# Optimization experiments

Measured on AMD Instinct MI355X. Metric: run time of the kernel, lower is better.

Reference implementation:

```python
import jax, jax.numpy as jnp
import numpy as np

HIDDEN = 768
HEADS = 12
HEAD_DIM = HIDDEN // HEADS


def setup_inputs() -> dict:
    key = jax.random.key(0)
    ks = jax.random.split(key, 9)
    B, S = 2, 2048
    scale = 1.0 / np.sqrt(HIDDEN)
    return {
        "hidden_states": jax.random.normal(ks[0], (B, S, HIDDEN), jnp.float32),
        "context": jax.random.normal(ks[1], (B, S, HIDDEN), jnp.float32),
        "attention_mask": jnp.zeros((B, 1, 1, S), jnp.float32),
        "Wq": jax.random.normal(ks[2], (HIDDEN, HIDDEN), jnp.float32) * scale,
        "bq": jnp.zeros((HIDDEN,), jnp.float32),
        "Wk": jax.random.normal(ks[3], (HIDDEN, HIDDEN), jnp.float32) * scale,
        "bk": jnp.zeros((HIDDEN,), jnp.float32),
        "Wv": jax.random.normal(ks[4], (HIDDEN, HIDDEN), jnp.float32) * scale,
        "bv": jnp.zeros((HIDDEN,), jnp.float32),
    }


def _split_heads(x):
    # [B, S, H*D] -> [B, H, S, D]
    B, S, _ = x.shape
    return x.reshape(B, S, HEADS, HEAD_DIM).transpose(0, 2, 1, 3)


def reference(hidden_states, context, attention_mask, Wq, bq, Wk, bk, Wv, bv):
    # torch Linear: y = x @ W^T + b
    q = _split_heads(hidden_states @ Wq.T + bq)   # [B,H,Sq,D]
    k = _split_heads(context @ Wk.T + bk)         # [B,H,Sk,D]
    v = _split_heads(context @ Wv.T + bv)         # [B,H,Sk,D]

    scores = jnp.einsum("bhqd,bhkd->bhqk", q, k)
    scores = scores / np.sqrt(HEAD_DIM + 1e-05)
    scores = scores + attention_mask
    probs = jax.nn.softmax(scores, axis=-1)       # dropout p=0 -> identity (eval)
    ctx = jnp.einsum("bhqk,bhkd->bhqd", probs, v) # [B,H,Sq,D]
    B, H, Sq, D = ctx.shape
    return ctx.transpose(0, 2, 1, 3).reshape(B, Sq, H * D)
```

## Files before the change

### kernel.cpp

```cpp
#include <hip/hip_runtime.h>
#include <hip/hip_bf16.h>
#include <math.h>

typedef short s16x8 __attribute__((ext_vector_type(8)));
typedef float f32x4 __attribute__((ext_vector_type(4)));
typedef _Float16 f16x4 __attribute__((ext_vector_type(4)));
typedef __fp16 fp16x2 __attribute__((ext_vector_type(2)));
typedef unsigned short u16;

#define NHEADS 12
#define SEQ 2048
#define NBH 24
#define KDIM 768
#define LOG2E 1.44269504088896f

#define SWZ(row, col) (((row) * 64) + ((col) ^ (((row) & 7) << 3)))

#define GLOAD_LDS16(g, l) __builtin_amdgcn_global_load_lds( \
    (const __attribute__((address_space(1))) unsigned int*)(g), \
    (__attribute__((address_space(3))) unsigned int*)(l), 16, 0, 0)

static __device__ __forceinline__ u16 f2bf(float f) {
    union { float f; unsigned u; } v; v.f = f;
    unsigned r = v.u + 0x7fffu + ((v.u >> 16) & 1u);
    return (u16)(r >> 16);
}
static __device__ __forceinline__ u16 f2h(float f) {
    union { _Float16 h; u16 u; } v; v.h = (_Float16)f;
    return v.u;
}
static __device__ __forceinline__ f16x4 pack4(float a, float b, float c, float d) {
    union { fp16x2 h2[2]; f16x4 h4; } u;
    u.h2[0] = __builtin_amdgcn_cvt_pkrtz(a, b);
    u.h2[1] = __builtin_amdgcn_cvt_pkrtz(c, d);
    return u.h4;
}

__global__ void cvt6_kernel(const float* __restrict__ s0, const float* __restrict__ s1,
                            const float* __restrict__ s2, const float* __restrict__ s3,
                            const float* __restrict__ s4, const float* __restrict__ s5,
                            u16* __restrict__ d0, u16* __restrict__ d1, u16* __restrict__ d2,
                            u16* __restrict__ d3, u16* __restrict__ d4, float* __restrict__ d5,
                            int n4a, int n4w, float qscl) {
    const int z = blockIdx.z;
    int i = blockIdx.x * blockDim.x + threadIdx.x;
    if (z == 5) {
        if (i < (2 * SEQ) / 4) {
            float4 f = ((const float4*)s5)[i];
            f.x *= LOG2E; f.y *= LOG2E; f.z *= LOG2E; f.w *= LOG2E;
            ((float4*)d5)[i] = f;
        }
        return;
    }
    const float* src = (z == 0) ? s0 : (z == 1) ? s1 : (z == 2) ? s2 : (z == 3) ? s3 : s4;
    u16* dst         = (z == 0) ? d0 : (z == 1) ? d1 : (z == 2) ? d2 : (z == 3) ? d3 : d4;
    const int n4     = (z < 2) ? n4a : n4w;
    const float scl  = (z == 2) ? qscl : 1.0f;
    if (i < n4) {
        float4 f = ((const float4*)src)[i];
        ushort4 o;
        o.x = f2bf(f.x * scl); o.y = f2bf(f.y * scl); o.z = f2bf(f.z * scl); o.w = f2bf(f.w * scl);
        ((ushort4*)dst)[i] = o;
    }
}

__launch_bounds__(256)
__global__ void qkv_gemm(const u16* __restrict__ X, const u16* __restrict__ C,
                         const u16* __restrict__ W0, const u16* __restrict__ W1, const u16* __restrict__ W2,
                         const float* __restrict__ b0, const float* __restrict__ b1, const float* __restrict__ b2,
                         u16* __restrict__ Qo, u16* __restrict__ Ko, u16* __restrict__ Vo, float qscl) {
    const int z = blockIdx.z;
    const u16* A    = (z == 0) ? X  : C;
    const u16* W    = (z == 0) ? W0 : (z == 1) ? W1 : W2;
    const float* bi = (z == 0) ? b0 : (z == 1) ? b1 : b2;
    u16* out        = (z == 0) ? Qo : (z == 1) ? Ko : Vo;
    const float bscl = (z == 0) ? qscl : 1.0f;

    __shared__ u16 As[3][4096];
    __shared__ u16 Bs[3][4096];

    const int tid  = threadIdx.x;
    const int lane = tid & 63;
    const int wid  = tid >> 6;
    const int wr = wid >> 1, wc = wid & 1;
    const int l15 = lane & 15, lh = lane >> 4;
    const int mBase = blockIdx.x * 128;
    const int nBase = blockIdx.y * 128;

    size_t aSrc[2], bSrc[2]; int ldsOff[2];
    #pragma unroll
    for (int i = 0; i < 2; ++i) {
        int L = i * 2048 + tid * 8;
        int prow = L >> 6;
        int pcol = (L & 63) ^ ((prow & 7) << 3);
        int row = (prow << 1) | (pcol >> 5);
        int col = pcol & 31;
        aSrc[i] = (size_t)(mBase + row) * KDIM + col;
        bSrc[i] = (size_t)(nBase + row) * KDIM + col;
        ldsOff[i] = i * 2048 + wid * 512;
    }

#define G_STAGE(step, buf) do { \
        const size_t kb_ = (size_t)(step) * 32; \
        GLOAD_LDS16(&A[aSrc[0] + kb_], &As[buf][ldsOff[0]]); \
        GLOAD_LDS16(&A[aSrc[1] + kb_], &As[buf][ldsOff[1]]); \
        GLOAD_LDS16(&W[bSrc[0] + kb_], &Bs[buf][ldsOff[0]]); \
        GLOAD_LDS16(&W[bSrc[1] + kb_], &Bs[buf][ldsOff[1]]); \
    } while (0)

    f32x4 acc[4][4] = {};

    G_STAGE(0, 0);
    G_STAGE(1, 1);

    const int NIT = KDIM / 32;
    int cur = 0;
    for (int it = 0; it < NIT; ++it) {
        if (it + 1 < NIT) asm volatile("s_waitcnt vmcnt(4)" ::: "memory");
        else              asm volatile("s_waitcnt vmcnt(0)" ::: "memory");
        __builtin_amdgcn_s_barrier();
        __builtin_amdgcn_sched_barrier(0);

        s16x8 xf[4], wf[4];
        #pragma unroll
        for (int m = 0; m < 4; ++m) {
            int row = wr * 64 + m * 16 + l15;
            xf[m] = *(const s16x8*)(&As[cur][SWZ(row >> 1, (row & 1) * 32 + lh * 8)]);
        }
        #pragma unroll
        for (int n = 0; n < 4; ++n) {
            int row = wc * 64 + n * 16 + l15;
            wf[n] = *(const s16x8*)(&Bs[cur][SWZ(row >> 1, (row & 1) * 32 + lh * 8)]);
        }
        if (z < 2) {
            #pragma unroll
            for (int m = 0; m < 4; ++m)
                #pragma unroll
                for (int n = 0; n < 4; ++n)
                    acc[m][n] = __builtin_amdgcn_mfma_f32_16x16x32_bf16(wf[n], xf[m], acc[m][n], 0, 0, 0);
        } else {
            #pragma unroll
            for (int m = 0; m < 4; ++m)
                #pragma unroll
                for (int n = 0; n < 4; ++n)
                    acc[m][n] = __builtin_amdgcn_mfma_f32_16x16x32_bf16(xf[m], wf[n], acc[m][n], 0, 0, 0);
        }

        if (it + 2 < NIT) {
            int nxt = cur + 2; if (nxt >= 3) nxt -= 3;
            G_STAGE(it + 2, nxt);
        }
        ++cur; if (cur == 3) cur = 0;
    }
#undef G_STAGE

    if (z < 2) {
        #pragma unroll
        for (int m = 0; m < 4; ++m) {
            int sg = mBase + wr * 64 + m * 16 + l15;
            int b = sg >> 11, s = sg & 2047;
            #pragma unroll
            for (int n = 0; n < 4; ++n) {
                int d0 = nBase + wc * 64 + n * 16 + lh * 4;
                int h = d0 >> 6, d = d0 & 63;
                float4 bv = *(const float4*)(&bi[d0]);
                ushort4 o;
                o.x = f2bf(acc[m][n][0] + bv.x * bscl);
                o.y = f2bf(acc[m][n][1] + bv.y * bscl);
                o.z = f2bf(acc[m][n][2] + bv.z * bscl);
                o.w = f2bf(acc[m][n][3] + bv.w * bscl);
                *(ushort4*)(&out[(((size_t)(b * NHEADS + h) * SEQ + s) << 6) + d]) = o;
            }
        }
    } else {
        #pragma unroll
        for (int m = 0; m < 4; ++m) {
            #pragma unroll
            for (int n = 0; n < 4; ++n) {
                int colg = nBase + wc * 64 + n * 16 + l15;
                float bv = bi[colg];
                int h = colg >> 6, d = colg & 63;
                int rowg0 = mBase + wr * 64 + m * 16 + lh * 4;
                int b = rowg0 >> 11, s = rowg0 & 2047;
                int sp = (s & ~0x3C) | (((s >> 2) & 3) << 4) | (((s >> 4) & 3) << 2);
                ushort4 o;
                o.x = f2h(acc[m][n][0] + bv);
                o.y = f2h(acc[m][n][1] + bv);
                o.z = f2h(acc[m][n][2] + bv);
                o.w = f2h(acc[m][n][3] + bv);
                *(ushort4*)(&out[(((size_t)(b * NHEADS + h) * 64 + d) << 11) + sp]) = o;
            }
        }
    }
}

template<bool SPLIT>
__launch_bounds__(512)
__global__ void attn_kernel(const u16* __restrict__ Qg, const u16* __restrict__ Kg,
                            const u16* __restrict__ Vg,
                            const float* __restrict__ maskL, float* __restrict__ out,
                            u16* __restrict__ OpartH, float* __restrict__ MLpart) {
    __shared__ u16 Ks[2][64 * 64];
    __shared__ u16 Vt[2][64 * 64];
    __shared__ float maskLds[2048];

    const int tid  = threadIdx.x;
    const int lane = tid & 63;
    const int wid  = tid >> 6;
    const int bh = blockIdx.y;
    const int b = bh / NHEADS;
    const int h = bh % NHEADS;
    const int q0 = blockIdx.x * 128 + wid * 16;
    const int l15 = lane & 15, lh = lane >> 4;
    const int z = SPLIT ? blockIdx.z : 0;
    const int NT = SPLIT ? (SEQ / 128) : (SEQ / 64);
    const int tile0 = z * NT;

    for (int i = tid * 4; i < NT * 64; i += 512 * 4)
        *(float4*)(&maskLds[i]) = *(const float4*)(&maskL[(size_t)b * SEQ + (tile0 << 6) + i]);

    const int srow = tid >> 3;
    const int scol = ((tid & 7) * 8) ^ ((srow & 7) << 3);
    const size_t kSrc = (((size_t)bh * SEQ + srow) << 6) + scol + ((size_t)tile0 << 12);
    const size_t vSrc = (((size_t)bh * 64 + srow) << 11) + scol + (size_t)tile0 * 64;
    const int ldsBase = wid * 512;

    s16x8 qf[2];
    #pragma unroll
    for (int kk = 0; kk < 2; ++kk)
        qf[kk] = *(const s16x8*)(&Qg[(((size_t)bh * SEQ + q0 + l15) << 6) + kk * 32 + lh * 8]);

    f32x4 oacc[4] = {};
    float mrun = -1e30f, lrun = 0.f;

    GLOAD_LDS16(&Kg[kSrc], &Ks[0][ldsBase]);
    GLOAD_LDS16(&Vg[vSrc], &Vt[0][ldsBase]);

    for (int t = 0; t < NT; ++t) {
        const int cur = t & 1;
        __syncthreads();
        if (t + 1 < NT) {
            GLOAD_LDS16(&Kg[kSrc + ((size_t)(t + 1) << 12)], &Ks[cur ^ 1][ldsBase]);
            GLOAD_LDS16(&Vg[vSrc + (size_t)(t + 1) * 64],    &Vt[cur ^ 1][ldsBase]);
        }

        f32x4 sacc[4];
        #pragma unroll
        for (int n = 0; n < 4; ++n) {
            float4 mv = *(const float4*)(&maskLds[t * 64 + n * 16 + lh * 4]);
            sacc[n][0] = mv.x; sacc[n][1] = mv.y; sacc[n][2] = mv.z; sacc[n][3] = mv.w;
        }
        __builtin_amdgcn_s_setprio(1);
        #pragma unroll
        for (int kk = 0; kk < 2; ++kk) {
            #pragma unroll
            for (int n = 0; n < 4; ++n) {
                s16x8 kf = *(const s16x8*)(&Ks[cur][SWZ(n * 16 + l15, kk * 32 + lh * 8)]);
                sacc[n] = __builtin_amdgcn_mfma_f32_16x16x32_bf16(kf, qf[kk], sacc[n], 0, 0, 0);
            }
        }
        __builtin_amdgcn_s_setprio(0);

        float tmax = sacc[0][0];
        #pragma unroll
        for (int n = 0; n < 4; ++n)
            #pragma unroll
            for (int j = 0; j < 4; ++j)
                tmax = fmaxf(tmax, sacc[n][j]);

        if (!__all(tmax - mrun <= 11.0f)) {
            float rmax = fmaxf(tmax, __shfl_xor(tmax, 16));
            rmax = fmaxf(rmax, __shfl_xor(rmax, 32));
            float mnew = fmaxf(mrun, rmax);
            float alpha = __builtin_amdgcn_exp2f(mrun - mnew);
            lrun *= alpha;
            #pragma unroll
            for (int nd = 0; nd < 4; ++nd)
                #pragma unroll
                for (int j = 0; j < 4; ++j)
                    oacc[nd][j] *= alpha;
            mrun = mnew;
        }

        f16x4 pf[4];
        #pragma unroll
        for (int n = 0; n < 4; ++n) {
            float p0 = __builtin_amdgcn_exp2f(sacc[n][0] - mrun);
            float p1 = __builtin_amdgcn_exp2f(sacc[n][1] - mrun);
            float p2 = __builtin_amdgcn_exp2f(sacc[n][2] - mrun);
            float p3 = __builtin_amdgcn_exp2f(sacc[n][3] - mrun);
            lrun += (p0 + p1) + (p2 + p3);
            pf[n] = pack4(p0, p1, p2, p3);
        }

        __builtin_amdgcn_s_setprio(1);
        #pragma unroll
        for (int kk = 0; kk < 2; ++kk) {
            #pragma unroll
            for (int nd = 0; nd < 4; ++nd) {
                s16x8 v2 = *(const s16x8*)(&Vt[cur][SWZ(nd * 16 + l15, lh * 16 + kk * 8)]);
                union { s16x8 s8; f16x4 h4[2]; } u; u.s8 = v2;
                oacc[nd] = __builtin_amdgcn_mfma_f32_16x16x16f16(u.h4[0], pf[2 * kk],     oacc[nd], 0, 0, 0);
                oacc[nd] = __builtin_amdgcn_mfma_f32_16x16x16f16(u.h4[1], pf[2 * kk + 1], oacc[nd], 0, 0, 0);
            }
        }
        __builtin_amdgcn_s_setprio(0);
    }

    lrun += __shfl_xor(lrun, 16);
    lrun += __shfl_xor(lrun, 32);

    const float inv = 1.0f / lrun;
    const int s = q0 + l15;
    if (!SPLIT) {
        #pragma unroll
        for (int nd = 0; nd < 4; ++nd) {
            float4 o;
            o.x = oacc[nd][0] * inv; o.y = oacc[nd][1] * inv;
            o.z = oacc[nd][2] * inv; o.w = oacc[nd][3] * inv;
            *(float4*)(&out[(size_t)(b * SEQ + s) * (NHEADS * 64) + h * 64 + nd * 16 + lh * 4]) = o;
        }
    } else {
        const size_t rbase = ((size_t)(z * NBH + bh) * SEQ + s);
        #pragma unroll
        for (int nd = 0; nd < 4; ++nd) {
            union { f16x4 h4; ushort4 u4; } o;
            o.h4 = pack4(oacc[nd][0] * inv, oacc[nd][1] * inv,
                         oacc[nd][2] * inv, oacc[nd][3] * inv);
            *(ushort4*)(&OpartH[rbase * 64 + nd * 16 + lh * 4]) = o.u4;
        }
        if (lh == 0)
            *(float2*)(&MLpart[rbase * 2]) = make_float2(mrun, lrun);
    }
}

__global__ void combine_kernel(const u16* __restrict__ OpartH, const float* __restrict__ MLpart,
                               float* __restrict__ out) {
    int gid = blockIdx.x * 256 + threadIdx.x;
    int row = gid >> 4, d4 = gid & 15;
    float2 ml0 = ((const float2*)MLpart)[row];
    float2 ml1 = ((const float2*)MLpart)[NBH * SEQ + row];
    float m = fmaxf(ml0.x, ml1.x);
    float w0 = __builtin_amdgcn_exp2f(ml0.x - m) * ml0.y;
    float w1 = __builtin_amdgcn_exp2f(ml1.x - m) * ml1.y;
    float inv = 1.0f / (w0 + w1);
    w0 *= inv; w1 *= inv;
    union { ushort4 u4; f16x4 h4; } a, c;
    a.u4 = *(const ushort4*)(&OpartH[(size_t)row * 64 + d4 * 4]);
    c.u4 = *(const ushort4*)(&OpartH[(size_t)NBH * SEQ * 64 + (size_t)row * 64 + d4 * 4]);
    float4 o;
    o.x = (float)a.h4[0] * w0 + (float)c.h4[0] * w1;
    o.y = (float)a.h4[1] * w0 + (float)c.h4[1] * w1;
    o.z = (float)a.h4[2] * w0 + (float)c.h4[2] * w1;
    o.w = (float)a.h4[3] * w0 + (float)c.h4[3] * w1;
    int bh = row >> 11, s = row & 2047;
    int b = bh / NHEADS, hh = bh % NHEADS;
    *(float4*)(&out[(size_t)(b * SEQ + s) * (NHEADS * 64) + hh * 64 + d4 * 4]) = o;
}

extern "C" void kernel_launch(void* const* d_in, const int* in_sizes, int n_in,
                              void* d_out, int out_size, void* d_ws, size_t ws_size,
                              hipStream_t stream) {
    const float* hidden  = (const float*)d_in[0];
    const float* context = (const float*)d_in[1];
    const float* mask    = (const float*)d_in[2];
    const float* Wq = (const float*)d_in[3];
    const float* bq = (const float*)d_in[4];
    const float* Wk = (const float*)d_in[5];
    const float* bk = (const float*)d_in[6];
    const float* Wv = (const float*)d_in[7];
    const float* bv = (const float*)d_in[8];
    float* out = (float*)d_out;

    char* ws = (char*)d_ws;
    const size_t XSZ = (size_t)4096 * 768 * 2;
    const size_t WSZ = (size_t)768 * 768 * 2;
    u16* X16  = (u16*)(ws);
    u16* C16  = (u16*)(ws + XSZ);
    u16* W16q = (u16*)(ws + 2 * XSZ);
    u16* W16k = (u16*)(ws + 2 * XSZ + WSZ);
    u16* W16v = (u16*)(ws + 2 * XSZ + 2 * WSZ);
    u16* Q16  = (u16*)(ws + 2 * XSZ + 3 * WSZ);
    u16* K16  = (u16*)(ws + 3 * XSZ + 3 * WSZ);
    u16* V16  = (u16*)(ws + 4 * XSZ + 3 * WSZ);
    const size_t MASKL_OFF = 5 * XSZ + 3 * WSZ;
    float* maskL = (float*)(ws + MASKL_OFF);
    const size_t OPART_OFF = MASKL_OFF + 2 * SEQ * sizeof(float) + 256;
    u16* OpartH = (u16*)(ws + OPART_OFF);
    const size_t ML_OFF = OPART_OFF + (size_t)2 * NBH * SEQ * 64 * 2;
    float* MLpart = (float*)(ws + ML_OFF);
    const size_t WS_NEED_SPLIT = ML_OFF + (size_t)2 * NBH * SEQ * 2 * 4;

    const float qscl = (float)((1.0 / sqrt(64.0 + 1e-5)) * 1.44269504088896);

    const int n4x = 4096 * 768 / 4;
    const int n4w = 768 * 768 / 4;
    cvt6_kernel<<<dim3((n4x + 255) / 256, 1, 6), 256, 0, stream>>>(
        hidden, context, Wq, Wk, Wv, mask,
        X16, C16, W16q, W16k, W16v, maskL, n4x, n4w, qscl);

    qkv_gemm<<<dim3(4096 / 128, 768 / 128, 3), 256, 0, stream>>>(
        X16, C16, W16q, W16k, W16v, bq, bk, bv, Q16, K16, V16, qscl);

    if (ws_size >= WS_NEED_SPLIT) {
        attn_kernel<true><<<dim3(SEQ / 128, NBH, 2), 512, 0, stream>>>(
            Q16, K16, V16, maskL, out, OpartH, MLpart);
        combine_kernel<<<(NBH * SEQ * 16) / 256, 256, 0, stream>>>(OpartH, MLpart, out);
    } else {
        attn_kernel<false><<<dim3(SEQ / 128, NBH, 1), 512, 0, stream>>>(
            Q16, K16, V16, maskL, out, OpartH, MLpart);
    }
}
```

Before: 93.41 us.

## Split attention KV range four ways with XCD-aware block remapping

Raises the flash-decoding style KV split from 2 to 4 partitions, generalizes the combine kernel to merge NSPL partial outputs, and adds a block-index remap so blocks sharing the same (batch, head, split) land on the same XCD for L2 reuse of K/V. The aim is more blocks in flight (1536 vs 768) to fill the 256 CUs, plus better L2 locality. In exchange it doubles the fp16 partial-output traffic and makes the combine kernel do more work.

```diff
diff --git a/kernel.cpp b/kernel.cpp
--- a/kernel.cpp
+++ b/kernel.cpp
@@ -12,6 +12,7 @@
 #define SEQ 2048
 #define NBH 24
 #define KDIM 768
+#define NSPL 4
 #define LOG2E 1.44269504088896f
 
 #define SWZ(row, col) (((row) * 64) + ((col) ^ (((row) & 7) << 3)))
@@ -194,26 +195,36 @@
     }
 }
 
-template<bool SPLIT>
+template<int NSPLIT>
 __launch_bounds__(512)
 __global__ void attn_kernel(const u16* __restrict__ Qg, const u16* __restrict__ Kg,
                             const u16* __restrict__ Vg,
                             const float* __restrict__ maskL, float* __restrict__ out,
                             u16* __restrict__ OpartH, float* __restrict__ MLpart) {
+    constexpr int NT = SEQ / 64 / NSPLIT;
     __shared__ u16 Ks[2][64 * 64];
     __shared__ u16 Vt[2][64 * 64];
-    __shared__ float maskLds[2048];
+    __shared__ float maskLds[NT * 64];
 
     const int tid  = threadIdx.x;
     const int lane = tid & 63;
     const int wid  = tid >> 6;
-    const int bh = blockIdx.y;
+
+    int qx, bh, z;
+    if (NSPLIT == 4) {
+        int L = blockIdx.x + 16 * (blockIdx.y + NBH * blockIdx.z);
+        int xcd = L & 7, idx = L >> 3;
+        int grp = xcd * 12 + (idx >> 4);
+        qx = idx & 15;
+        bh = grp % NBH;
+        z  = grp / NBH;
+    } else {
+        qx = blockIdx.x; bh = blockIdx.y; z = 0;
+    }
     const int b = bh / NHEADS;
     const int h = bh % NHEADS;
-    const int q0 = blockIdx.x * 128 + wid * 16;
+    const int q0 = qx * 128 + wid * 16;
     const int l15 = lane & 15, lh = lane >> 4;
-    const int z = SPLIT ? blockIdx.z : 0;
-    const int NT = SPLIT ? (SEQ / 128) : (SEQ / 64);
     const int tile0 = z * NT;
 
     for (int i = tid * 4; i < NT * 64; i += 512 * 4)
@@ -312,7 +323,7 @@
 
     const float inv = 1.0f / lrun;
     const int s = q0 + l15;
-    if (!SPLIT) {
+    if (NSPLIT == 1) {
         #pragma unroll
         for (int nd = 0; nd < 4; ++nd) {
             float4 o;
@@ -338,21 +349,29 @@
                                float* __restrict__ out) {
     int gid = blockIdx.x * 256 + threadIdx.x;
     int row = gid >> 4, d4 = gid & 15;
-    float2 ml0 = ((const float2*)MLpart)[row];
-    float2 ml1 = ((const float2*)MLpart)[NBH * SEQ + row];
-    float m = fmaxf(ml0.x, ml1.x);
-    float w0 = __builtin_amdgcn_exp2f(ml0.x - m) * ml0.y;
-    float w1 = __builtin_amdgcn_exp2f(ml1.x - m) * ml1.y;
-    float inv = 1.0f / (w0 + w1);
-    w0 *= inv; w1 *= inv;
-    union { ushort4 u4; f16x4 h4; } a, c;
-    a.u4 = *(const ushort4*)(&OpartH[(size_t)row * 64 + d4 * 4]);
-    c.u4 = *(const ushort4*)(&OpartH[(size_t)NBH * SEQ * 64 + (size_t)row * 64 + d4 * 4]);
-    float4 o;
-    o.x = (float)a.h4[0] * w0 + (float)c.h4[0] * w1;
-    o.y = (float)a.h4[1] * w0 + (float)c.h4[1] * w1;
-    o.z = (float)a.h4[2] * w0 + (float)c.h4[2] * w1;
-    o.w = (float)a.h4[3] * w0 + (float)c.h4[3] * w1;
+    float2 ml[NSPL];
+    float m = -1e30f;
+    #pragma unroll
+    for (int k = 0; k < NSPL; ++k) {
+        ml[k] = ((const float2*)MLpart)[(size_t)k * NBH * SEQ + row];
+        m = fmaxf(m, ml[k].x);
+    }
+    float w[NSPL], wsum = 0.f;
+    #pragma unroll
+    for (int k = 0; k < NSPL; ++k) {
+        w[k] = __builtin_amdgcn_exp2f(ml[k].x - m) * ml[k].y;
+        wsum += w[k];
+    }
+    float inv = 1.0f / wsum;
+    float4 o = {0.f, 0.f, 0.f, 0.f};
+    #pragma unroll
+    for (int k = 0; k < NSPL; ++k) {
+        union { ushort4 u4; f16x4 h4; } a;
+        a.u4 = *(const ushort4*)(&OpartH[((size_t)k * NBH * SEQ + row) * 64 + d4 * 4]);
+        float wk = w[k] * inv;
+        o.x += (float)a.h4[0] * wk; o.y += (float)a.h4[1] * wk;
+        o.z += (float)a.h4[2] * wk; o.w += (float)a.h4[3] * wk;
+    }
     int bh = row >> 11, s = row & 2047;
     int b = bh / NHEADS, hh = bh % NHEADS;
     *(float4*)(&out[(size_t)(b * SEQ + s) * (NHEADS * 64) + hh * 64 + d4 * 4]) = o;
@@ -387,9 +406,9 @@
     float* maskL = (float*)(ws + MASKL_OFF);
     const size_t OPART_OFF = MASKL_OFF + 2 * SEQ * sizeof(float) + 256;
     u16* OpartH = (u16*)(ws + OPART_OFF);
-    const size_t ML_OFF = OPART_OFF + (size_t)2 * NBH * SEQ * 64 * 2;
+    const size_t ML_OFF = OPART_OFF + (size_t)NSPL * NBH * SEQ * 64 * 2;
     float* MLpart = (float*)(ws + ML_OFF);
-    const size_t WS_NEED_SPLIT = ML_OFF + (size_t)2 * NBH * SEQ * 2 * 4;
+    const size_t WS_NEED_SPLIT = ML_OFF + (size_t)NSPL * NBH * SEQ * 2 * 4;
 
     const float qscl = (float)((1.0 / sqrt(64.0 + 1e-5)) * 1.44269504088896);
 
@@ -403,11 +422,11 @@
         X16, C16, W16q, W16k, W16v, bq, bk, bv, Q16, K16, V16, qscl);
 
     if (ws_size >= WS_NEED_SPLIT) {
-        attn_kernel<true><<<dim3(SEQ / 128, NBH, 2), 512, 0, stream>>>(
+        attn_kernel<NSPL><<<dim3(SEQ / 128, NBH, NSPL), 512, 0, stream>>>(
             Q16, K16, V16, maskL, out, OpartH, MLpart);
         combine_kernel<<<(NBH * SEQ * 16) / 256, 256, 0, stream>>>(OpartH, MLpart, out);
     } else {
-        attn_kernel<false><<<dim3(SEQ / 128, NBH, 1), 512, 0, stream>>>(
+        attn_kernel<1><<<dim3(SEQ / 128, NBH, 1), 512, 0, stream>>>(
             Q16, K16, V16, maskL, out, OpartH, MLpart);
     }
 }
```

New measurement: 97.05 us. +3.9%, slower.
